# Kernel optimization log

Hardware: AMD Instinct MI355X
Metric: run time of the kernel (lower is better)

The kernel has to match this reference:

```python
import jax, jax.numpy as jnp
import numpy as np

# Geometry (matches init_kwargs)
B, C, N_DET, N_T = 4, 1, 128, 1024
NX, NY = 256, 256
DT = 2.5e-8          # 40 MHz sampling
PITCH = 0.0003       # 0.3 mm element pitch
C_SOUND = 1540.0
X0, DX = -0.01905, 0.00015
Y0, DY = 0.0, 0.0001
ARR_X0, ARR_Y = -0.01905, 0.0
N_FFT = N_T          # fft_pad = 0


def setup_inputs() -> dict:
    key = jax.random.key(0)
    sino = jax.random.normal(key, (B, C, N_DET, N_T), dtype=jnp.float32)

    # Frequency axis and rfft Parseval-style weighting
    freq = np.fft.rfftfreq(N_FFT, d=DT).astype(np.float32)
    omega = (2.0 * np.pi * freq).astype(np.float32)          # [n_f]
    w = np.ones_like(omega)
    if omega.size > 2:
        w[1:-1] = 2.0
    if N_FFT % 2 == 0 and omega.size > 1:
        w[-1] = 1.0

    # Lateral wavenumbers and image coordinates
    kx = (2.0 * np.pi * np.fft.fftfreq(N_DET, d=PITCH)).astype(np.float32)  # [n_det]
    xs = X0 + np.arange(NX, dtype=np.float32) * DX
    ys = Y0 + np.arange(NY, dtype=np.float32) * DY
    x_phase = xs - ARR_X0
    y_phase = ys - ARR_Y

    # Dispersion relation: kz^2 = (omega/c)^2 - kx^2 ; evanescent mask
    kz_sq = (omega / C_SOUND)[None, :] ** 2 - (kx ** 2)[:, None]          # [n_det, n_f]
    prop_mask = (kz_sq > 0).astype(np.float32)
    kz = np.sqrt(np.clip(kz_sq, 0.0, None)).astype(np.float32)

    phase_x = np.exp(1j * (kx[:, None] * x_phase[None, :])).astype(np.complex64)        # [n_det, nx]
    phase_y = np.exp(1j * (y_phase[:, None, None] * kz[None, :, :])).astype(np.complex64)  # [ny, n_det, n_f]

    time_window = np.ones(N_T, dtype=np.float32)  # window=None -> rectangular
    apod = (0.5 - 0.5 * np.cos(2.0 * np.pi * np.arange(N_DET) / max(N_DET - 1, 1))).astype(np.float32)

    return {
        "sino": sino,
        "time_window": jnp.asarray(time_window),
        "apod": jnp.asarray(apod),
        "freq_weight": jnp.asarray(w),
        "prop_mask": jnp.asarray(prop_mask),
        "phase_x": jnp.asarray(phase_x),
        "phase_y": jnp.asarray(phase_y),
    }


def reference(sino, time_window, apod, freq_weight, prop_mask, phase_x, phase_y):
    # Per-sample normalization over (n_det, n_t)
    eps = jnp.finfo(sino.dtype).eps
    mean = sino.mean(axis=(-1, -2), keepdims=True)
    centered = sino - mean
    std = jnp.sqrt((centered * centered).mean(axis=(-1, -2), keepdims=True) + eps)
    x = (centered / std) * time_window[None, None, None, :] * apod[None, None, :, None]

    # Time rfft then detector fft -> P(kx, omega)
    spec = jnp.fft.rfft(x, n=N_FFT, axis=-1)          # [B,C,n_det,n_f]
    skf = jnp.fft.fft(spec, axis=-2)                  # [B,C,n_kx,n_f]

    # Evanescent mask + one-sided spectrum weighting
    skf = skf * (prop_mask * freq_weight[None, :])[None, None].astype(skf.dtype)

    # Inverse extrapolation: sum_f e^{i kz y}, then sum_kx e^{i kx x}
    tmp = jnp.einsum('bcdf,ydf->bcyd', skf, phase_y)  # [B,C,ny,n_kx]
    img = jnp.einsum('bcyd,dx->bcyx', tmp, phase_x)   # [B,C,ny,nx]

    n_det = sino.shape[2]
    return img.real / (n_det * freq_weight.sum())
```

## Files before the change

kernel.cpp:

```cpp
#include <hip/hip_runtime.h>
#include <math.h>

#define NDET 128
#define NT   1024
#define NF   513
#define NB   4
#define NXI  256
#define NYI  256
#define NCH  8

#define KX_STEP 163.62462f
#define OC_STEP 159.37463f
#define DY_F 1.0e-4f
#define DX_F 1.5e-4f

__device__ __forceinline__ void bfly(float2& a, float2& b, float cw, float sw) {
    float tr = b.x * cw - b.y * sw;
    float ti = b.x * sw + b.y * cw;
    b.x = a.x - tr; b.y = a.y - ti;
    a.x += tr;      a.y += ti;
}

__global__ __launch_bounds__(256) void k_fft_time(
        const float* __restrict__ sino, const float* __restrict__ tw,
        const float* __restrict__ apod, float* __restrict__ part,
        float2* __restrict__ spec) {
    __shared__ float2 X[1024];
    int tid = threadIdx.x;
    int blk = blockIdx.x;
    if (blk >= 512) {
        float* s1 = (float*)X;
        float* s2 = s1 + 256;
        int sb = blk - 512;
        const float4* p = (const float4*)sino + (size_t)sb * 1024;
        float s = 0.f, q = 0.f;
#pragma unroll
        for (int i = 0; i < 4; ++i) {
            float4 v = p[tid + i * 256];
            s += v.x + v.y + v.z + v.w;
            q += v.x * v.x + v.y * v.y + v.z * v.z + v.w * v.w;
        }
        s1[tid] = s; s2[tid] = q; __syncthreads();
        for (int off = 128; off > 0; off >>= 1) {
            if (tid < off) { s1[tid] += s1[tid + off]; s2[tid] += s2[tid + off]; }
            __syncthreads();
        }
        if (tid == 0) { part[sb] = s1[0]; part[128 + sb] = s2[0]; }
        return;
    }
    int row = blk;
    int d = row & 127;
    float ap = apod[d];
    const float4* p4 = (const float4*)(sino + (size_t)row * NT);
    const float4* w4 = (const float4*)tw;
    float4 v4 = p4[tid];
    float4 t4 = w4[tid];
    int t0 = tid * 4;
    X[__brev((unsigned)(t0 + 0)) >> 22] = make_float2(v4.x * t4.x * ap, 0.f);
    X[__brev((unsigned)(t0 + 1)) >> 22] = make_float2(v4.y * t4.y * ap, 0.f);
    X[__brev((unsigned)(t0 + 2)) >> 22] = make_float2(v4.z * t4.z * ap, 0.f);
    X[__brev((unsigned)(t0 + 3)) >> 22] = make_float2(v4.w * t4.w * ap, 0.f);
    __syncthreads();
    for (int s = 1; s <= 10; ++s) {
        int half = 1 << (s - 1);
        for (int j = tid; j < 512; j += 256) {
            int grp = j >> (s - 1);
            int pos = j & (half - 1);
            int i1 = (grp << s) + pos;
            int i2 = i1 + half;
            float ang = -6.28318530718f * (float)pos / (float)(2 * half);
            float sw, cw; __sincosf(ang, &sw, &cw);
            bfly(X[i1], X[i2], cw, sw);
        }
        __syncthreads();
    }
    float2* out = spec + (size_t)row * NF;
    for (int f = tid; f < NF; f += 256) out[f] = X[f];
}

__global__ __launch_bounds__(256) void k_fft_det(
        const float2* __restrict__ spec, const float* __restrict__ pm,
        const float* __restrict__ fw, float2* __restrict__ wskf) {
    __shared__ float2 Xs[8][128];
    int tid = threadIdx.x;
    int b  = blockIdx.x / 65;
    int f0 = (blockIdx.x % 65) * 8;
    for (int l = tid; l < 1024; l += 256) {
        int j = l & 7, d = l >> 3;
        int f = f0 + j;
        float2 v = make_float2(0.f, 0.f);
        if (f < NF) v = spec[((size_t)(b * NDET + d)) * NF + f];
        Xs[j][__brev((unsigned)d) >> 25] = v;
    }
    __syncthreads();
    for (int s = 1; s <= 7; ++s) {
        int half = 1 << (s - 1);
        for (int l = tid; l < 512; l += 256) {
            int r = l >> 6, q = l & 63;
            int grp = q >> (s - 1), pos = q & (half - 1);
            int i1 = (grp << s) + pos, i2 = i1 + half;
            float ang = -6.28318530718f * (float)pos / (float)(2 * half);
            float sw, cw; __sincosf(ang, &sw, &cw);
            bfly(Xs[r][i1], Xs[r][i2], cw, sw);
        }
        __syncthreads();
    }
    for (int l = tid; l < 1024; l += 256) {
        int j = l & 7, k = l >> 3;
        int f = f0 + j;
        if (f < NF) {
            float mw = pm[k * NF + f] * fw[f];
            float2 v = Xs[j][k];
            wskf[((size_t)(b * NDET + k)) * NF + f] = make_float2(v.x * mw, v.y * mw);
        }
    }
}

__global__ __launch_bounds__(256) void k_prop(const float2* __restrict__ wskf,
                                              float2* __restrict__ tmpP) {
    __shared__ float  kzs[65];
    __shared__ float2 skA[4][65];
    __shared__ float2 skB[4][65];
    int tid = threadIdx.x;
    int p = blockIdx.x >> 3;
    int c = blockIdx.x & 7;
    int f_start = c * 64;
    int nf = (c == 7) ? 65 : 64;
    int kA = p;
    int kB = (128 - p) & 127;
    bool hasB = (p >= 1 && p <= 63);
    float kxv = (float)p * KX_STEP;
    float kx2 = kxv * kxv;
    for (int i = tid; i < nf; i += 256) {
        float oc = (float)(f_start + i) * OC_STEP;
        float d2 = oc * oc - kx2;
        kzs[i] = d2 > 0.f ? sqrtf(d2) : 0.f;
    }
#pragma unroll
    for (int bb = 0; bb < NB; ++bb) {
        for (int i = tid; i < nf; i += 256) {
            skA[bb][i] = wskf[((size_t)(bb * NDET + kA)) * NF + f_start + i];
            skB[bb][i] = hasB ? wskf[((size_t)(bb * NDET + kB)) * NF + f_start + i]
                              : make_float2(0.f, 0.f);
        }
    }
    __syncthreads();
    int y = tid;
    float yp = (float)y * DY_F;
    float aAr[4] = {0,0,0,0}, aAi[4] = {0,0,0,0};
    float aBr[4] = {0,0,0,0}, aBi[4] = {0,0,0,0};
    for (int i = 0; i < nf; ++i) {
        float sw, cw; __sincosf(yp * kzs[i], &sw, &cw);
#pragma unroll
        for (int bb = 0; bb < 4; ++bb) {
            float2 vA = skA[bb][i];
            aAr[bb] += vA.x * cw - vA.y * sw;  aAi[bb] += vA.x * sw + vA.y * cw;
            float2 vB = skB[bb][i];
            aBr[bb] += vB.x * cw - vB.y * sw;  aBi[bb] += vB.x * sw + vB.y * cw;
        }
    }
    size_t cb = (size_t)c * NB * NDET;
#pragma unroll
    for (int bb = 0; bb < 4; ++bb) {
        tmpP[(cb + bb * NDET + kA) * NYI + y] = make_float2(aAr[bb], aAi[bb]);
        if (hasB)
            tmpP[(cb + bb * NDET + kB) * NYI + y] = make_float2(aBr[bb], aBi[bb]);
    }
}

__global__ __launch_bounds__(256) void k_img(const float2* __restrict__ tmpP,
                                             const float* __restrict__ part,
                                             float* __restrict__ outp) {
    __shared__ float2 ts[2][128];
    __shared__ float sred[4];
    int tid = threadIdx.x;
    int y  = blockIdx.x >> 1;
    int bh = blockIdx.x & 1;
    if (tid < 128) {
        int g = tid >> 5, lane = tid & 31;
        int bb = 2 * bh + (g >> 1);
        int which = g & 1;
        float v = part[which * 128 + bb * 32 + lane];
        for (int off = 16; off > 0; off >>= 1) v += __shfl_down(v, off);
        if (lane == 0) sred[g] = v;
    }
    int bl = tid >> 7;
    int k  = tid & 127;
    float2 a = make_float2(0.f, 0.f);
#pragma unroll
    for (int cc = 0; cc < NCH; ++cc) {
        float2 v = tmpP[(((size_t)cc * NB + 2 * bh + bl) * NDET + k) * NYI + y];
        a.x += v.x; a.y += v.y;
    }
    ts[bl][k] = a;
    __syncthreads();
    const float inv_n = 1.0f / 131072.0f;
    float m0 = sred[0] * inv_n;
    float v0 = sred[1] * inv_n - m0 * m0;
    float m1 = sred[2] * inv_n;
    float v1 = sred[3] * inv_n - m1 * m1;
    float sc0 = inv_n / sqrtf(v0 + 1.1920929e-7f);
    float sc1 = inv_n / sqrtf(v1 + 1.1920929e-7f);
    float alpha = KX_STEP * (float)tid * DX_F;
    float sa, ca; __sincosf(alpha, &sa, &ca);
    float acc0 = ts[0][0].x, acc1 = ts[1][0].x;
    float c = ca, s = sa;
    for (int p = 1; p <= 63; ++p) {
        float2 tp0 = ts[0][p], tm0 = ts[0][128 - p];
        acc0 += c * (tp0.x + tm0.x) - s * (tp0.y - tm0.y);
        float2 tp1 = ts[1][p], tm1 = ts[1][128 - p];
        acc1 += c * (tp1.x + tm1.x) - s * (tp1.y - tm1.y);
        float nc = c * ca - s * sa;
        s = s * ca + c * sa;
        c = nc;
    }
    float2 t640 = ts[0][64], t641 = ts[1][64];
    acc0 += c * t640.x + s * t640.y;
    acc1 += c * t641.x + s * t641.y;
    outp[((size_t)(2 * bh + 0) * NYI + y) * NXI + tid] = acc0 * sc0;
    outp[((size_t)(2 * bh + 1) * NYI + y) * NXI + tid] = acc1 * sc1;
}

extern "C" void kernel_launch(void* const* d_in, const int* in_sizes, int n_in,
                              void* d_out, int out_size, void* d_ws, size_t ws_size,
                              hipStream_t stream) {
    const float* sino = (const float*)d_in[0];
    const float* tw   = (const float*)d_in[1];
    const float* apod = (const float*)d_in[2];
    const float* fw   = (const float*)d_in[3];
    const float* pm   = (const float*)d_in[4];

    float*  wsf   = (float*)d_ws;
    float*  part  = wsf;
    float2* spec  = (float2*)(wsf + 512);
    float2* wskf  = spec + (size_t)NB * NDET * NF;
    float2* tmpP  = wskf + (size_t)NB * NDET * NF;
    float*  outp  = (float*)d_out;

    k_fft_time<<<dim3(640), dim3(256), 0, stream>>>(sino, tw, apod, part, spec);
    k_fft_det <<<dim3(260), dim3(256), 0, stream>>>(spec, pm, fw, wskf);
    k_prop    <<<dim3(520), dim3(256), 0, stream>>>(wskf, tmpP);
    k_img     <<<dim3(512), dim3(256), 0, stream>>>(tmpP, part, outp);
}
```

Measured before the change: 57.97 us.

## Fuse stats into time FFT, pad LDS, rebalance det FFT and prop grids

The per-sample sum and sum-of-squares reduction moves out of its 128 extra blocks and into the time-FFT blocks, using wave shuffles that write per-row partials, which k_img then reduces. The time-FFT shared buffer gets a padding index to reduce LDS bank conflicts. The detector FFT uses 4 frequencies per block (512 blocks) instead of 8 (260 blocks). k_prop drops its p=0 idle half by pairing kx=0 with kx=64, giving 512 balanced blocks instead of 520 with some half-idle. Costs are an extra sincos for p=0 and more partials to read in k_img.

```diff
diff --git a/kernel.cpp b/kernel.cpp
--- a/kernel.cpp
+++ b/kernel.cpp
@@ -21,127 +21,125 @@
     a.x += tr;      a.y += ti;
 }
 
+__device__ __forceinline__ int ax(int i) { return i + (i >> 4); }
+
 __global__ __launch_bounds__(256) void k_fft_time(
         const float* __restrict__ sino, const float* __restrict__ tw,
         const float* __restrict__ apod, float* __restrict__ part,
         float2* __restrict__ spec) {
-    __shared__ float2 X[1024];
-    int tid = threadIdx.x;
-    int blk = blockIdx.x;
-    if (blk >= 512) {
-        float* s1 = (float*)X;
-        float* s2 = s1 + 256;
-        int sb = blk - 512;
-        const float4* p = (const float4*)sino + (size_t)sb * 1024;
-        float s = 0.f, q = 0.f;
-#pragma unroll
-        for (int i = 0; i < 4; ++i) {
-            float4 v = p[tid + i * 256];
-            s += v.x + v.y + v.z + v.w;
-            q += v.x * v.x + v.y * v.y + v.z * v.z + v.w * v.w;
-        }
-        s1[tid] = s; s2[tid] = q; __syncthreads();
-        for (int off = 128; off > 0; off >>= 1) {
-            if (tid < off) { s1[tid] += s1[tid + off]; s2[tid] += s2[tid + off]; }
-            __syncthreads();
-        }
-        if (tid == 0) { part[sb] = s1[0]; part[128 + sb] = s2[0]; }
-        return;
-    }
-    int row = blk;
+    __shared__ float2 X[1088];
+    __shared__ float sw4[4], qw4[4];
+    int tid = threadIdx.x;
+    int row = blockIdx.x;
     int d = row & 127;
     float ap = apod[d];
     const float4* p4 = (const float4*)(sino + (size_t)row * NT);
     const float4* w4 = (const float4*)tw;
     float4 v4 = p4[tid];
     float4 t4 = w4[tid];
+    float s = v4.x + v4.y + v4.z + v4.w;
+    float q = v4.x * v4.x + v4.y * v4.y + v4.z * v4.z + v4.w * v4.w;
+#pragma unroll
+    for (int off = 32; off > 0; off >>= 1) {
+        s += __shfl_down(s, off);
+        q += __shfl_down(q, off);
+    }
+    if ((tid & 63) == 0) { sw4[tid >> 6] = s; qw4[tid >> 6] = q; }
     int t0 = tid * 4;
-    X[__brev((unsigned)(t0 + 0)) >> 22] = make_float2(v4.x * t4.x * ap, 0.f);
-    X[__brev((unsigned)(t0 + 1)) >> 22] = make_float2(v4.y * t4.y * ap, 0.f);
-    X[__brev((unsigned)(t0 + 2)) >> 22] = make_float2(v4.z * t4.z * ap, 0.f);
-    X[__brev((unsigned)(t0 + 3)) >> 22] = make_float2(v4.w * t4.w * ap, 0.f);
-    __syncthreads();
-    for (int s = 1; s <= 10; ++s) {
-        int half = 1 << (s - 1);
+    X[ax(__brev((unsigned)(t0 + 0)) >> 22)] = make_float2(v4.x * t4.x * ap, 0.f);
+    X[ax(__brev((unsigned)(t0 + 1)) >> 22)] = make_float2(v4.y * t4.y * ap, 0.f);
+    X[ax(__brev((unsigned)(t0 + 2)) >> 22)] = make_float2(v4.z * t4.z * ap, 0.f);
+    X[ax(__brev((unsigned)(t0 + 3)) >> 22)] = make_float2(v4.w * t4.w * ap, 0.f);
+    __syncthreads();
+    if (tid == 0) {
+        part[row]       = sw4[0] + sw4[1] + sw4[2] + sw4[3];
+        part[512 + row] = qw4[0] + qw4[1] + qw4[2] + qw4[3];
+    }
+    for (int st = 1; st <= 10; ++st) {
+        int half = 1 << (st - 1);
         for (int j = tid; j < 512; j += 256) {
-            int grp = j >> (s - 1);
+            int grp = j >> (st - 1);
             int pos = j & (half - 1);
-            int i1 = (grp << s) + pos;
+            int i1 = (grp << st) + pos;
             int i2 = i1 + half;
             float ang = -6.28318530718f * (float)pos / (float)(2 * half);
-            float sw, cw; __sincosf(ang, &sw, &cw);
-            bfly(X[i1], X[i2], cw, sw);
+            float sn, cs; __sincosf(ang, &sn, &cs);
+            bfly(X[ax(i1)], X[ax(i2)], cs, sn);
         }
         __syncthreads();
     }
     float2* out = spec + (size_t)row * NF;
-    for (int f = tid; f < NF; f += 256) out[f] = X[f];
+    for (int f = tid; f < NF; f += 256) out[f] = X[ax(f)];
 }
 
 __global__ __launch_bounds__(256) void k_fft_det(
         const float2* __restrict__ spec, const float* __restrict__ pm,
         const float* __restrict__ fw, float2* __restrict__ wskf) {
-    __shared__ float2 Xs[8][128];
-    int tid = threadIdx.x;
-    int b  = blockIdx.x / 65;
-    int f0 = (blockIdx.x % 65) * 8;
-    for (int l = tid; l < 1024; l += 256) {
-        int j = l & 7, d = l >> 3;
-        int f = f0 + j;
-        float2 v = make_float2(0.f, 0.f);
-        if (f < NF) v = spec[((size_t)(b * NDET + d)) * NF + f];
-        Xs[j][__brev((unsigned)d) >> 25] = v;
-    }
-    __syncthreads();
-    for (int s = 1; s <= 7; ++s) {
-        int half = 1 << (s - 1);
-        for (int l = tid; l < 512; l += 256) {
-            int r = l >> 6, q = l & 63;
-            int grp = q >> (s - 1), pos = q & (half - 1);
-            int i1 = (grp << s) + pos, i2 = i1 + half;
+    __shared__ float2 Xs[5][128];
+    int tid = threadIdx.x;
+    int b  = blockIdx.x >> 7;
+    int fg = blockIdx.x & 127;
+    int rows = (fg == 127) ? 5 : 4;
+    int f0 = fg * 4;
+    for (int l = tid; l < 512; l += 256) {
+        int j = l & 3, dd = l >> 2;
+        Xs[j][__brev((unsigned)dd) >> 25] = spec[((size_t)(b * NDET + dd)) * NF + f0 + j];
+    }
+    if (rows == 5 && tid < 128)
+        Xs[4][__brev((unsigned)tid) >> 25] = spec[((size_t)(b * NDET + tid)) * NF + 512];
+    __syncthreads();
+    for (int st = 1; st <= 7; ++st) {
+        int half = 1 << (st - 1);
+        for (int l = tid; l < rows * 64; l += 256) {
+            int r = l >> 6, qq = l & 63;
+            int grp = qq >> (st - 1), pos = qq & (half - 1);
+            int i1 = (grp << st) + pos, i2 = i1 + half;
             float ang = -6.28318530718f * (float)pos / (float)(2 * half);
-            float sw, cw; __sincosf(ang, &sw, &cw);
-            bfly(Xs[r][i1], Xs[r][i2], cw, sw);
+            float sn, cs; __sincosf(ang, &sn, &cs);
+            bfly(Xs[r][i1], Xs[r][i2], cs, sn);
         }
         __syncthreads();
     }
-    for (int l = tid; l < 1024; l += 256) {
-        int j = l & 7, k = l >> 3;
-        int f = f0 + j;
-        if (f < NF) {
-            float mw = pm[k * NF + f] * fw[f];
-            float2 v = Xs[j][k];
-            wskf[((size_t)(b * NDET + k)) * NF + f] = make_float2(v.x * mw, v.y * mw);
-        }
+    for (int l = tid; l < 512; l += 256) {
+        int j = l & 3, k = l >> 2;
+        float mw = pm[k * NF + f0 + j] * fw[f0 + j];
+        float2 v = Xs[j][k];
+        wskf[((size_t)(b * NDET + k)) * NF + f0 + j] = make_float2(v.x * mw, v.y * mw);
+    }
+    if (rows == 5 && tid < 128) {
+        int k = tid;
+        float mw = pm[k * NF + 512] * fw[512];
+        float2 v = Xs[4][k];
+        wskf[((size_t)(b * NDET + k)) * NF + 512] = make_float2(v.x * mw, v.y * mw);
     }
 }
 
 __global__ __launch_bounds__(256) void k_prop(const float2* __restrict__ wskf,
                                               float2* __restrict__ tmpP) {
-    __shared__ float  kzs[65];
-    __shared__ float2 skA[4][65];
-    __shared__ float2 skB[4][65];
+    __shared__ float  kzA[65], kzB[65];
+    __shared__ float2 skA[4][65], skB[4][65];
     int tid = threadIdx.x;
     int p = blockIdx.x >> 3;
     int c = blockIdx.x & 7;
     int f_start = c * 64;
     int nf = (c == 7) ? 65 : 64;
     int kA = p;
-    int kB = (128 - p) & 127;
-    bool hasB = (p >= 1 && p <= 63);
-    float kxv = (float)p * KX_STEP;
-    float kx2 = kxv * kxv;
+    int kB = (p == 0) ? 64 : 128 - p;
+    float kxA = (float)p * KX_STEP;
+    float kxB = (p == 0) ? 64.0f * KX_STEP : kxA;
+    float kxA2 = kxA * kxA, kxB2 = kxB * kxB;
     for (int i = tid; i < nf; i += 256) {
         float oc = (float)(f_start + i) * OC_STEP;
-        float d2 = oc * oc - kx2;
-        kzs[i] = d2 > 0.f ? sqrtf(d2) : 0.f;
+        float o2 = oc * oc;
+        float dA = o2 - kxA2, dB = o2 - kxB2;
+        kzA[i] = dA > 0.f ? sqrtf(dA) : 0.f;
+        kzB[i] = dB > 0.f ? sqrtf(dB) : 0.f;
     }
 #pragma unroll
     for (int bb = 0; bb < NB; ++bb) {
         for (int i = tid; i < nf; i += 256) {
             skA[bb][i] = wskf[((size_t)(bb * NDET + kA)) * NF + f_start + i];
-            skB[bb][i] = hasB ? wskf[((size_t)(bb * NDET + kB)) * NF + f_start + i]
-                              : make_float2(0.f, 0.f);
+            skB[bb][i] = wskf[((size_t)(bb * NDET + kB)) * NF + f_start + i];
         }
     }
     __syncthreads();
@@ -149,22 +147,25 @@
     float yp = (float)y * DY_F;
     float aAr[4] = {0,0,0,0}, aAi[4] = {0,0,0,0};
     float aBr[4] = {0,0,0,0}, aBi[4] = {0,0,0,0};
+    bool p0 = (p == 0);
     for (int i = 0; i < nf; ++i) {
-        float sw, cw; __sincosf(yp * kzs[i], &sw, &cw);
+        float snA, csA; __sincosf(yp * kzA[i], &snA, &csA);
+        float snB, csB;
+        if (p0) { __sincosf(yp * kzB[i], &snB, &csB); }
+        else    { snB = snA; csB = csA; }
 #pragma unroll
         for (int bb = 0; bb < 4; ++bb) {
             float2 vA = skA[bb][i];
-            aAr[bb] += vA.x * cw - vA.y * sw;  aAi[bb] += vA.x * sw + vA.y * cw;
+            aAr[bb] += vA.x * csA - vA.y * snA;  aAi[bb] += vA.x * snA + vA.y * csA;
             float2 vB = skB[bb][i];
-            aBr[bb] += vB.x * cw - vB.y * sw;  aBi[bb] += vB.x * sw + vB.y * cw;
+            aBr[bb] += vB.x * csB - vB.y * snB;  aBi[bb] += vB.x * snB + vB.y * csB;
         }
     }
     size_t cb = (size_t)c * NB * NDET;
 #pragma unroll
     for (int bb = 0; bb < 4; ++bb) {
         tmpP[(cb + bb * NDET + kA) * NYI + y] = make_float2(aAr[bb], aAi[bb]);
-        if (hasB)
-            tmpP[(cb + bb * NDET + kB) * NYI + y] = make_float2(aBr[bb], aBi[bb]);
+        tmpP[(cb + bb * NDET + kB) * NYI + y] = make_float2(aBr[bb], aBi[bb]);
     }
 }
 
@@ -176,12 +177,14 @@
     int tid = threadIdx.x;
     int y  = blockIdx.x >> 1;
     int bh = blockIdx.x & 1;
-    if (tid < 128) {
-        int g = tid >> 5, lane = tid & 31;
+    {
+        int g = tid >> 6, lane = tid & 63;
         int bb = 2 * bh + (g >> 1);
         int which = g & 1;
-        float v = part[which * 128 + bb * 32 + lane];
-        for (int off = 16; off > 0; off >>= 1) v += __shfl_down(v, off);
+        float v = part[which * 512 + bb * 128 + lane] +
+                  part[which * 512 + bb * 128 + 64 + lane];
+#pragma unroll
+        for (int off = 32; off > 0; off >>= 1) v += __shfl_down(v, off);
         if (lane == 0) sred[g] = v;
     }
     int bl = tid >> 7;
@@ -227,18 +230,18 @@
     const float* sino = (const float*)d_in[0];
     const float* tw   = (const float*)d_in[1];
     const float* apod = (const float*)d_in[2];
+    const float* pm   = (const float*)d_in[4];
     const float* fw   = (const float*)d_in[3];
-    const float* pm   = (const float*)d_in[4];
 
     float*  wsf   = (float*)d_ws;
     float*  part  = wsf;
-    float2* spec  = (float2*)(wsf + 512);
+    float2* spec  = (float2*)(wsf + 1024);
     float2* wskf  = spec + (size_t)NB * NDET * NF;
     float2* tmpP  = wskf + (size_t)NB * NDET * NF;
     float*  outp  = (float*)d_out;
 
-    k_fft_time<<<dim3(640), dim3(256), 0, stream>>>(sino, tw, apod, part, spec);
-    k_fft_det <<<dim3(260), dim3(256), 0, stream>>>(spec, pm, fw, wskf);
-    k_prop    <<<dim3(520), dim3(256), 0, stream>>>(wskf, tmpP);
+    k_fft_time<<<dim3(512), dim3(256), 0, stream>>>(sino, tw, apod, part, spec);
+    k_fft_det <<<dim3(512), dim3(256), 0, stream>>>(spec, pm, fw, wskf);
+    k_prop    <<<dim3(512), dim3(256), 0, stream>>>(wskf, tmpP);
     k_img     <<<dim3(512), dim3(256), 0, stream>>>(tmpP, part, outp);
 }
```

New measurement: 53.45 us. -7.8%, faster.
